# Performance work log

Measured on AMD Instinct MI355X. Metric: run time of the kernel, lower is better.

Reference implementation:

```python
import jax, jax.numpy as jnp
import numpy as np

B = 2048
S = 8            # mem_slots
H = 8            # num_heads
HS = 128         # head_size
KS = 128         # key_size (= head_size)
VS = 128         # value_size
M = H * HS       # mem_size = 1024
QKV = 2 * KS + VS            # 384
TOTAL = QKV * H              # 3072
IN_DIM = 1024
NUM_GATES = 2                # gate_style='memory' -> gate size 1, x2 gates
FORGET_BIAS = 1.0
INPUT_BIAS = 0.0


def _glorot(key, shape):
    fan_in, fan_out = shape[0], shape[1]
    lim = np.sqrt(6.0 / (fan_in + fan_out))
    return jax.random.uniform(key, shape, jnp.float32, -lim, lim)


def setup_inputs() -> dict:
    key = jax.random.key(0)
    ks = jax.random.split(key, 16)
    return {
        "inputs": jax.random.normal(ks[0], (B, IN_DIM), jnp.float32),
        "memory": jax.random.normal(ks[1], (B, S * M), jnp.float32),
        "kernel_qkv": _glorot(ks[2], (M, TOTAL)),
        "bias_qkv": jnp.zeros((TOTAL,), jnp.float32),
        "kernel_gi": _glorot(ks[3], (M, NUM_GATES)),
        "bias_gi": _glorot(ks[4], (1, NUM_GATES))[0],
        "kernel_gm": _glorot(ks[5], (M, NUM_GATES)),
        "bias_gm": _glorot(ks[6], (1, NUM_GATES))[0],
        "kernel_in": _glorot(ks[7], (IN_DIM, M)),
        "bias_in": _glorot(ks[8], (1, M))[0],
        "mlp_k0": _glorot(ks[9], (M, M)),
        "mlp_b0": _glorot(ks[10], (1, M))[0],
        "mlp_k1": _glorot(ks[11], (M, M)),
        "mlp_b1": _glorot(ks[12], (1, M))[0],
    }


def reference(inputs, memory, kernel_qkv, bias_qkv, kernel_gi, bias_gi,
              kernel_gm, bias_gm, kernel_in, bias_in,
              mlp_k0, mlp_b0, mlp_k1, mlp_b1):
    b = inputs.shape[0]
    mem = memory.reshape(b, S, M)                       # (B, S, M)
    x = inputs @ kernel_in + bias_in                    # (B, M)
    mpi = jnp.concatenate([mem, x[:, None, :]], axis=1)  # (B, S+1, M)

    # multi-head attention over memory + input slot
    qkv = (mpi @ kernel_qkv + bias_qkv).reshape(b, S + 1, H, QKV)
    qkv = qkv.transpose(0, 2, 1, 3)                     # (B, H, S+1, QKV)
    q = qkv[..., :KS] * (QKV ** -0.5)
    k = qkv[..., KS:2 * KS]
    v = qkv[..., 2 * KS:]
    w = jax.nn.softmax(jnp.einsum('bhqd,bhkd->bhqk', q, k), axis=-1)
    att = jnp.einsum('bhqk,bhkd->bhqd', w, v)           # (B, H, S+1, VS)
    att = att.transpose(0, 2, 1, 3).reshape(b, S + 1, M)
    m1 = mpi + att                                      # residual attention

    # residual 2-layer MLP (relu between layers)
    h = jax.nn.relu(m1 @ mlp_k0 + mlp_b0)
    m2 = m1 + (h @ mlp_k1 + mlp_b1)

    nxt = m2[:, :-1, :]                                 # drop input slot

    # per-slot (memory-style) gates
    gi = (x @ kernel_gi + bias_gi)[:, None, :]          # (B, 1, 2)
    gm = jnp.tanh(mem) @ kernel_gm + bias_gm            # (B, S, 2)
    gates = gm + gi
    input_gate = jax.nn.sigmoid(gates[..., :1] + INPUT_BIAS)
    forget_gate = jax.nn.sigmoid(gates[..., 1:] + FORGET_BIAS)

    nxt = input_gate * jnp.tanh(nxt) + forget_gate * mem
    return nxt.reshape(b, S * M)
```

## Files before the change

### kernel.cpp

```cpp
#include <hip/hip_runtime.h>
#include <math.h>


typedef unsigned short ushort_t;
typedef short bf16x8_t __attribute__((ext_vector_type(8)));
typedef float f32x4_t  __attribute__((ext_vector_type(4)));

#define MFMA16(a, b, c) __builtin_amdgcn_mfma_f32_16x16x32_bf16((a), (b), (c), 0, 0, 0)
#define SCHED_PIN() __builtin_amdgcn_sched_barrier(0)

__device__ __forceinline__ ushort_t f2bf(float f) {
    unsigned int u = __float_as_uint(f);
    u += 0x7fff + ((u >> 16) & 1);
    return (ushort_t)(u >> 16);
}
__device__ __forceinline__ float bf2f(ushort_t h) {
    return __uint_as_float(((unsigned int)h) << 16);
}
__device__ __forceinline__ float fast_tanh(float x) {
    float e = __expf(2.0f * x);
    return 1.0f - 2.0f * __builtin_amdgcn_rcpf(e + 1.0f);
}
__device__ __forceinline__ float fast_sigmoid(float x) {
    return __builtin_amdgcn_rcpf(1.0f + __expf(-x));
}

__device__ __forceinline__ void load_lds_16(const void* g, void* l) {
    __builtin_amdgcn_global_load_lds(
        (const __attribute__((address_space(1))) void*)g,
        (__attribute__((address_space(3))) void*)l, 16, 0, 0);
}

__global__ __launch_bounds__(512, 2)
void gemm256(const ushort_t* __restrict__ A, const ushort_t* __restrict__ Wt,
             const float* __restrict__ bias, ushort_t* __restrict__ Cb,
             const ushort_t* __restrict__ resb, const float* __restrict__ igfg,
             const ushort_t* __restrict__ memb, float* __restrict__ outp,
             int N, int K, int relu, int ncol, int nrow)
{
    __shared__ __align__(16) ushort_t As[2][256][64];
    __shared__ __align__(16) ushort_t Bs[2][256][64];

    const int tid   = threadIdx.x;
    const int wave  = tid >> 6, lane = tid & 63;
    const int lrow  = lane & 15, lquad = lane >> 4;
    const int wr    = (wave >> 2) * 64;
    const int wc    = (wave & 3) * 32;

    const int nwg = ncol * nrow;
    int l = blockIdx.x;
    int q = nwg >> 3, r = nwg & 7;
    int xcd = l & 7, ib = l >> 3;
    int wg = (xcd < r) ? xcd * (q + 1) + ib : r * (q + 1) + (xcd - r) * q + ib;
    int rT = wg / ncol, cT = wg - rT * ncol;
    const int rowBase = rT * 256;
    const int colBase = cT * 256;

    const int NT = K >> 6;

    auto stage = [&](const ushort_t* __restrict__ G, int gbase, int kt,
                     int half, ushort_t (*lds)[64]) {
        #pragma unroll
        for (int j = 0; j < 2; ++j) {
            int ci   = j * 512 + tid;
            int rl   = ci >> 3;
            int slot = ci & 7;
            int row  = half * 128 + rl;
            int gc   = slot ^ (rl & 7);
            const ushort_t* g = G + (size_t)(gbase + row) * K + kt * 64 + gc * 8;
            load_lds_16(g, &lds[row][slot * 8]);
        }
    };

    stage(A,  rowBase, 0, 0, As[0]);
    stage(A,  rowBase, 0, 1, As[0]);
    stage(Wt, colBase, 0, 0, Bs[0]);
    stage(Wt, colBase, 0, 1, Bs[0]);
    asm volatile("" ::: "memory");
    stage(A,  rowBase, 1, 0, As[1]);
    stage(Wt, colBase, 1, 0, Bs[1]);
    asm volatile("s_waitcnt vmcnt(4)" ::: "memory");
    SCHED_PIN();
    __builtin_amdgcn_s_barrier();
    SCHED_PIN();

    f32x4_t acc[8][4] = {};
    bf16x8_t af[4][2], bfr[4][2];
    const int s0 = (lquad ^ (lrow & 7)) * 8;
    const int s1 = ((lquad ^ (lrow & 7)) ^ 4) * 8;

    for (int t = 0; t < NT; ++t) {
        const int bf = t & 1, nf = bf ^ 1;
        ushort_t (*Ab)[64] = As[bf];
        ushort_t (*Bb)[64] = Bs[bf];

        #pragma unroll
        for (int m = 0; m < 4; ++m) {
            int ra = wr + m * 16 + lrow;
            af[m][0] = *(const bf16x8_t*)&Ab[ra][s0];
            af[m][1] = *(const bf16x8_t*)&Ab[ra][s1];
        }
        #pragma unroll
        for (int n = 0; n < 2; ++n) {
            int rb = wc + n * 16 + lrow;
            bfr[n][0] = *(const bf16x8_t*)&Bb[rb][s0];
            bfr[n][1] = *(const bf16x8_t*)&Bb[rb][s1];
        }
        if (t + 1 < NT) stage(A, rowBase, t + 1, 1, As[nf]);
        asm volatile("s_waitcnt lgkmcnt(8)" ::: "memory");
        SCHED_PIN();
        __builtin_amdgcn_s_barrier();
        asm volatile("s_waitcnt lgkmcnt(0)" ::: "memory");
        SCHED_PIN();
        __builtin_amdgcn_s_setprio(1);
        #pragma unroll
        for (int m = 0; m < 4; ++m)
            #pragma unroll
            for (int n = 0; n < 2; ++n) {
                acc[m][n] = MFMA16(af[m][0], bfr[n][0], acc[m][n]);
                acc[m][n] = MFMA16(af[m][1], bfr[n][1], acc[m][n]);
            }
        __builtin_amdgcn_s_setprio(0);
        SCHED_PIN();
        __builtin_amdgcn_s_barrier();
        SCHED_PIN();

        #pragma unroll
        for (int n = 0; n < 2; ++n) {
            int rb = 128 + wc + n * 16 + lrow;
            bfr[2 + n][0] = *(const bf16x8_t*)&Bb[rb][s0];
            bfr[2 + n][1] = *(const bf16x8_t*)&Bb[rb][s1];
        }
        if (t + 1 < NT) stage(Wt, colBase, t + 1, 1, Bs[nf]);
        SCHED_PIN();
        __builtin_amdgcn_s_barrier();
        asm volatile("s_waitcnt lgkmcnt(0)" ::: "memory");
        SCHED_PIN();
        __builtin_amdgcn_s_setprio(1);
        #pragma unroll
        for (int m = 0; m < 4; ++m)
            #pragma unroll
            for (int n = 0; n < 2; ++n) {
                acc[m][2 + n] = MFMA16(af[m][0], bfr[2 + n][0], acc[m][2 + n]);
                acc[m][2 + n] = MFMA16(af[m][1], bfr[2 + n][1], acc[m][2 + n]);
            }
        __builtin_amdgcn_s_setprio(0);
        SCHED_PIN();
        __builtin_amdgcn_s_barrier();
        SCHED_PIN();

        #pragma unroll
        for (int m = 0; m < 4; ++m) {
            int ra = 128 + wr + m * 16 + lrow;
            af[m][0] = *(const bf16x8_t*)&Ab[ra][s0];
            af[m][1] = *(const bf16x8_t*)&Ab[ra][s1];
        }
        if (t + 2 < NT) stage(A, rowBase, t + 2, 0, As[bf]);
        SCHED_PIN();
        __builtin_amdgcn_s_barrier();
        asm volatile("s_waitcnt lgkmcnt(0)" ::: "memory");
        SCHED_PIN();
        __builtin_amdgcn_s_setprio(1);
        #pragma unroll
        for (int m = 0; m < 4; ++m)
            #pragma unroll
            for (int n = 0; n < 2; ++n) {
                acc[4 + m][n] = MFMA16(af[m][0], bfr[n][0], acc[4 + m][n]);
                acc[4 + m][n] = MFMA16(af[m][1], bfr[n][1], acc[4 + m][n]);
            }
        __builtin_amdgcn_s_setprio(0);
        SCHED_PIN();
        __builtin_amdgcn_s_barrier();
        SCHED_PIN();

        if (t + 2 < NT) {
            stage(Wt, colBase, t + 2, 0, Bs[bf]);
            asm volatile("s_waitcnt vmcnt(4)" ::: "memory");
        } else if (t + 1 < NT) {
            asm volatile("s_waitcnt vmcnt(0)" ::: "memory");
        }
        SCHED_PIN();
        __builtin_amdgcn_s_barrier();
        SCHED_PIN();
        __builtin_amdgcn_s_setprio(1);
        #pragma unroll
        for (int m = 0; m < 4; ++m)
            #pragma unroll
            for (int n = 0; n < 2; ++n) {
                acc[4 + m][2 + n] = MFMA16(af[m][0], bfr[2 + n][0], acc[4 + m][2 + n]);
                acc[4 + m][2 + n] = MFMA16(af[m][1], bfr[2 + n][1], acc[4 + m][2 + n]);
            }
        __builtin_amdgcn_s_setprio(0);
        SCHED_PIN();
        __builtin_amdgcn_s_barrier();
        SCHED_PIN();
    }

    #pragma unroll
    for (int mi = 0; mi < 8; ++mi) {
        #pragma unroll
        for (int ni = 0; ni < 4; ++ni) {
            int col = colBase + wc + (ni & 1) * 16 + ((ni >> 1) << 7) + lrow;
            float bv = bias[col];
            #pragma unroll
            for (int rr = 0; rr < 4; ++rr) {
                int row = rowBase + wr + (mi & 3) * 16 + ((mi >> 2) << 7)
                        + lquad * 4 + rr;
                size_t idx = (size_t)row * N + col;
                float v = acc[mi][ni][rr] + bv;
                if (resb) v += bf2f(resb[idx]);
                if (relu) v = fmaxf(v, 0.f);
                if (outp) {
                    float ig = igfg[row * 2], fg = igfg[row * 2 + 1];
                    float mv = bf2f(memb[(size_t)(row + (row >> 3)) * N + col]);
                    outp[idx] = ig * fast_tanh(v) + fg * mv;
                } else {
                    Cb[idx] = f2bf(v);
                }
            }
        }
    }
}

__global__ __launch_bounds__(256)
void gemm_mfma(const ushort_t* __restrict__ A, const ushort_t* __restrict__ Wt,
               const float* __restrict__ bias, float* __restrict__ Cf,
               ushort_t* __restrict__ Cb, const ushort_t* __restrict__ resb,
               const float* __restrict__ igfg, const ushort_t* __restrict__ memb,
               float* __restrict__ outp, int N, int K, int relu,
               int ncol, int nrow)
{
    __shared__ __align__(16) ushort_t As[128 * 32];
    __shared__ __align__(16) ushort_t Bs[128 * 32];
    const int tid  = threadIdx.x;
    const int wave = tid >> 6, lane = tid & 63;
    const int wr = (wave >> 1) * 64;
    const int wc = (wave & 1)  * 64;
    const int lrow  = lane & 15;
    const int lquad = lane >> 4;

    int l = blockIdx.x, rT, cT;
    if ((nrow & 7) == 0) {
        int group = l / (8 * ncol);
        int w     = l - group * 8 * ncol;
        rT = group * 8 + (w & 7);
        cT = w >> 3;
    } else {
        rT = l / ncol;
        cT = l - rT * ncol;
    }
    const int rowBase = rT * 128;
    const int colBase = cT * 128;

    f32x4_t acc[4][4] = {};

    for (int k0 = 0; k0 < K; k0 += 32) {
        #pragma unroll
        for (int i = 0; i < 2; ++i) {
            int e    = i * 256 + tid;
            int row  = e >> 2;
            int c    = (e & 3) ^ ((row >> 1) & 3);
            const ushort_t* ga = A  + (size_t)(rowBase + row) * K + k0 + c * 8;
            const ushort_t* gb = Wt + (size_t)(colBase + row) * K + k0 + c * 8;
            load_lds_16(ga, &As[e * 8]);
            load_lds_16(gb, &Bs[e * 8]);
        }
        __syncthreads();

        bf16x8_t af[4], bfr[4];
        #pragma unroll
        for (int t = 0; t < 4; ++t) {
            int ma = wr + t * 16 + lrow;
            int pa = lquad ^ ((ma >> 1) & 3);
            af[t]  = *(const bf16x8_t*)&As[ma * 32 + pa * 8];
            int nb = wc + t * 16 + lrow;
            int pb = lquad ^ ((nb >> 1) & 3);
            bfr[t] = *(const bf16x8_t*)&Bs[nb * 32 + pb * 8];
        }
        #pragma unroll
        for (int mi = 0; mi < 4; ++mi)
            #pragma unroll
            for (int ni = 0; ni < 4; ++ni)
                acc[mi][ni] = MFMA16(af[mi], bfr[ni], acc[mi][ni]);
        __syncthreads();
    }

    #pragma unroll
    for (int mi = 0; mi < 4; ++mi) {
        #pragma unroll
        for (int ni = 0; ni < 4; ++ni) {
            int col = colBase + wc + ni * 16 + lrow;
            float bv = bias[col];
            #pragma unroll
            for (int r = 0; r < 4; ++r) {
                int row = rowBase + wr + mi * 16 + lquad * 4 + r;
                size_t idx = (size_t)row * N + col;
                float v = acc[mi][ni][r] + bv;
                if (resb) v += bf2f(resb[idx]);
                if (relu) v = fmaxf(v, 0.f);
                if (outp) {
                    float ig = igfg[row * 2], fg = igfg[row * 2 + 1];
                    float mv = bf2f(memb[(size_t)(row + (row >> 3)) * N + col]);
                    outp[idx] = ig * fast_tanh(v) + fg * mv;
                } else if (Cb) {
                    Cb[idx] = f2bf(v);
                } else {
                    Cf[idx] = v;
                }
            }
        }
    }
}

__global__ __launch_bounds__(256)
void conv_bf16(const float* __restrict__ in, ushort_t* __restrict__ out, size_t n)
{
    size_t i = ((size_t)blockIdx.x * 256 + threadIdx.x) * 4;
    if (i >= n) return;
    float4 v = *(const float4*)(in + i);
    out[i + 0] = f2bf(v.x); out[i + 1] = f2bf(v.y);
    out[i + 2] = f2bf(v.z); out[i + 3] = f2bf(v.w);
}

__global__ __launch_bounds__(256)
void conv_wt4(const float* __restrict__ W0, ushort_t* __restrict__ T0,
              const float* __restrict__ W1, ushort_t* __restrict__ T1,
              const float* __restrict__ W2, ushort_t* __restrict__ T2,
              const float* __restrict__ W3, ushort_t* __restrict__ T3)
{
    __shared__ float t[32][33];
    int bx = blockIdx.x;
    const float* W; ushort_t* T; int N;
    if (bx < 32)       { W = W0; T = T0; N = 1024; }
    else if (bx < 128) { W = W1; T = T1; N = 3072; bx -= 32; }
    else if (bx < 160) { W = W2; T = T2; N = 1024; bx -= 128; }
    else               { W = W3; T = T3; N = 1024; bx -= 160; }
    const int K = 1024;
    const int n0 = bx * 32, k0 = blockIdx.y * 32;
    const int tx = threadIdx.x & 31, ty = threadIdx.x >> 5;
    #pragma unroll
    for (int i = 0; i < 4; ++i)
        t[ty * 4 + i][tx] = W[(size_t)(k0 + ty * 4 + i) * N + n0 + tx];
    __syncthreads();
    #pragma unroll
    for (int i = 0; i < 4; ++i)
        T[(size_t)(n0 + ty * 4 + i) * K + k0 + tx] = f2bf(t[tx][ty * 4 + i]);
}

__global__ __launch_bounds__(256)
void prep_kernel(const float* __restrict__ mem, const ushort_t* __restrict__ xb,
                 const float* __restrict__ kgm, const float* __restrict__ bgm,
                 const float* __restrict__ gi, ushort_t* __restrict__ mpi,
                 float* __restrict__ igfg)
{
    const int row = blockIdx.x;
    const int tid = threadIdx.x;
    const int b = row / 9, s = row - b * 9;
    if (s == 8) {
        ((ushort4*)(mpi + (size_t)row * 1024))[tid] =
            ((const ushort4*)(xb + (size_t)b * 1024))[tid];
        return;
    }
    const float* mrow = mem + ((size_t)b * 8 + s) * 1024;
    float4 v = ((const float4*)mrow)[tid];
    ushort4 o;
    o.x = f2bf(v.x); o.y = f2bf(v.y); o.z = f2bf(v.z); o.w = f2bf(v.w);
    ((ushort4*)(mpi + (size_t)row * 1024))[tid] = o;
    float4 k0 = ((const float4*)kgm)[tid * 2];
    float4 k1 = ((const float4*)kgm)[tid * 2 + 1];
    float t0 = fast_tanh(v.x), t1 = fast_tanh(v.y);
    float t2 = fast_tanh(v.z), t3 = fast_tanh(v.w);
    float g0 = t0 * k0.x + t1 * k0.z + t2 * k1.x + t3 * k1.z;
    float g1 = t0 * k0.y + t1 * k0.w + t2 * k1.y + t3 * k1.w;
    #pragma unroll
    for (int m = 1; m <= 32; m <<= 1) {
        g0 += __shfl_xor(g0, m);
        g1 += __shfl_xor(g1, m);
    }
    __shared__ float wg[4][2];
    if ((tid & 63) == 0) { wg[tid >> 6][0] = g0; wg[tid >> 6][1] = g1; }
    __syncthreads();
    if (tid == 0) {
        float G0 = wg[0][0] + wg[1][0] + wg[2][0] + wg[3][0];
        float G1 = wg[0][1] + wg[1][1] + wg[2][1] + wg[3][1];
        int orow = b * 8 + s;
        igfg[orow * 2 + 0] = fast_sigmoid(G0 + bgm[0] + gi[b * 2 + 0]);
        igfg[orow * 2 + 1] = fast_sigmoid(G1 + bgm[1] + gi[b * 2 + 1] + 1.0f);
    }
}

__global__ __launch_bounds__(256)
void attn_kernel(const ushort_t* __restrict__ qkv, const ushort_t* __restrict__ mpib,
                 ushort_t* __restrict__ m1b)
{
    const int bh = blockIdx.x;
    const int b = bh >> 3, h = bh & 7;
    constexpr int VS = 40;
    __shared__ __align__(16) ushort_t vt[128 * VS];
    __shared__ __align__(16) ushort_t pw[16 * VS];
    const int tid  = threadIdx.x;
    const int lane = tid & 63, wave = tid >> 6;
    const int quad = lane >> 4;
    const size_t qrow0 = (size_t)b * 9;

    {
        unsigned long long* z = (unsigned long long*)vt;
        #pragma unroll
        for (int i = 0; i < 5; ++i) z[tid + i * 256] = 0ull;
        if (tid < 160) ((unsigned long long*)pw)[tid] = 0ull;
    }
    __syncthreads();
    for (int c = tid; c < 9 * 128; c += 256) {
        int j = c >> 7, d = c & 127;
        vt[d * VS + j] = qkv[(qrow0 + j) * 3072 + (size_t)h * 384 + 256 + d];
    }

    f32x4_t sacc = {0.f, 0.f, 0.f, 0.f};
    if (wave == 0) {
        const int m  = lane & 7;
        const int n  = lane & 15;
        const int nc = n > 8 ? 8 : n;
        const ushort_t* qb = qkv + (qrow0 + m)  * 3072 + (size_t)h * 384 + quad * 8;
        const ushort_t* kb = qkv + (qrow0 + nc) * 3072 + (size_t)h * 384 + 128 + quad * 8;
        #pragma unroll
        for (int t = 0; t < 4; ++t) {
            bf16x8_t aq = *(const bf16x8_t*)(qb + t * 32);
            bf16x8_t bk = *(const bf16x8_t*)(kb + t * 32);
            sacc = __builtin_amdgcn_mfma_f32_16x16x32_bf16(aq, bk, sacc, 0, 0, 0);
        }
    }
    __syncthreads();

    if (wave == 0) {
        const int j = lane & 15;
        const float scale = 0.05103103630798288f;
        #pragma unroll
        for (int r = 0; r < 4; ++r) {
            float sv = (j < 9) ? sacc[r] * scale : -1e30f;
            float mx = sv;
            mx = fmaxf(mx, __shfl_xor(mx, 1));
            mx = fmaxf(mx, __shfl_xor(mx, 2));
            mx = fmaxf(mx, __shfl_xor(mx, 4));
            mx = fmaxf(mx, __shfl_xor(mx, 8));
            float e = (j < 9) ? __expf(sv - mx) : 0.f;
            float sum = e;
            sum += __shfl_xor(sum, 1);
            sum += __shfl_xor(sum, 2);
            sum += __shfl_xor(sum, 4);
            sum += __shfl_xor(sum, 8);
            pw[(quad * 4 + r) * VS + j] = f2bf(e * __builtin_amdgcn_rcpf(sum));
        }
    }
    __syncthreads();

    {
        const int n  = lane & 15;
        const int d0 = wave * 32;
        bf16x8_t pa = *(const bf16x8_t*)&pw[n * VS + quad * 8];
        #pragma unroll
        for (int g = 0; g < 2; ++g) {
            int d = d0 + g * 16 + n;
            bf16x8_t vb = *(const bf16x8_t*)&vt[d * VS + quad * 8];
            f32x4_t o = {0.f, 0.f, 0.f, 0.f};
            o = __builtin_amdgcn_mfma_f32_16x16x32_bf16(pa, vb, o, 0, 0, 0);
            #pragma unroll
            for (int r = 0; r < 4; ++r) {
                int i = quad * 4 + r;
                if (i < 8) {
                    float mv = bf2f(mpib[((size_t)b * 9 + i) * 1024 + (size_t)h * 128 + d]);
                    size_t idx = ((size_t)b * 8 + i) * 1024 + (size_t)h * 128 + d;
                    m1b[idx] = f2bf(o[r] + mv);
                }
            }
        }
    }
}

__global__ __launch_bounds__(256)
void gi_kernel(const ushort_t* __restrict__ xb, const float* __restrict__ kgi,
               const float* __restrict__ bgi, float* __restrict__ gi)
{
    const int b = blockIdx.x, tid = threadIdx.x;
    float g0 = 0.f, g1 = 0.f;
    for (int k = tid; k < 1024; k += 256) {
        float xv = bf2f(xb[(size_t)b * 1024 + k]);
        g0 += xv * kgi[k * 2];
        g1 += xv * kgi[k * 2 + 1];
    }
    #pragma unroll
    for (int m = 1; m <= 32; m <<= 1) {
        g0 += __shfl_xor(g0, m);
        g1 += __shfl_xor(g1, m);
    }
    __shared__ float wg[4][2];
    if ((tid & 63) == 0) { wg[tid >> 6][0] = g0; wg[tid >> 6][1] = g1; }
    __syncthreads();
    if (tid == 0) {
        gi[b * 2 + 0] = wg[0][0] + wg[1][0] + wg[2][0] + wg[3][0] + bgi[0];
        gi[b * 2 + 1] = wg[0][1] + wg[1][1] + wg[2][1] + wg[3][1] + bgi[1];
    }
}

extern "C" void kernel_launch(void* const* d_in, const int* in_sizes, int n_in,
                              void* d_out, int out_size, void* d_ws, size_t ws_size,
                              hipStream_t stream)
{
    const float* inputs     = (const float*)d_in[0];
    const float* memory     = (const float*)d_in[1];
    const float* kernel_qkv = (const float*)d_in[2];
    const float* bias_qkv   = (const float*)d_in[3];
    const float* kernel_gi  = (const float*)d_in[4];
    const float* bias_gi    = (const float*)d_in[5];
    const float* kernel_gm  = (const float*)d_in[6];
    const float* bias_gm    = (const float*)d_in[7];
    const float* kernel_in  = (const float*)d_in[8];
    const float* bias_in    = (const float*)d_in[9];
    const float* mlp_k0     = (const float*)d_in[10];
    const float* mlp_b0     = (const float*)d_in[11];
    const float* mlp_k1     = (const float*)d_in[12];
    const float* mlp_b1     = (const float*)d_in[13];
    float* out = (float*)d_out;

    char* p = (char*)d_ws;
    ushort_t* in_b   = (ushort_t*)p;  p += (size_t)2048 * 1024 * 2;
    ushort_t* x_b    = (ushort_t*)p;  p += (size_t)2048 * 1024 * 2;
    ushort_t* wt_in  = (ushort_t*)p;  p += (size_t)1024 * 1024 * 2;
    ushort_t* wt_qkv = (ushort_t*)p;  p += (size_t)3072 * 1024 * 2;
    ushort_t* wt_k0  = (ushort_t*)p;  p += (size_t)1024 * 1024 * 2;
    ushort_t* wt_k1  = (ushort_t*)p;  p += (size_t)1024 * 1024 * 2;
    float*    ws_gi  = (float*)p;     p += (size_t)2048 * 2 * 4;
    float*    igfg   = (float*)p;     p += (size_t)16384 * 2 * 4;
    ushort_t* ws_mpi = (ushort_t*)p;  p += (size_t)18432 * 1024 * 2;
    ushort_t* m1b    = (ushort_t*)p;  p += (size_t)16384 * 1024 * 2;
    ushort_t* ws_h   = (ushort_t*)p;  p += (size_t)16384 * 1024 * 2;
    size_t fixed = (size_t)(p - (char*)d_ws);

    int Bc = 256;
    for (int cand = 1024; cand >= 256; cand >>= 1)
        if (fixed + (size_t)cand * 9 * 3072 * 2 <= ws_size) { Bc = cand; break; }
    ushort_t* ws_qkv = (ushort_t*)p;

    conv_bf16<<<2048, 256, 0, stream>>>(inputs, in_b, (size_t)2048 * 1024);
    conv_wt4<<<dim3(192, 32), 256, 0, stream>>>(
        kernel_in, wt_in, kernel_qkv, wt_qkv, mlp_k0, wt_k0, mlp_k1, wt_k1);

    gemm_mfma<<<16 * 8, 256, 0, stream>>>(
        in_b, wt_in, bias_in, nullptr, x_b, nullptr, nullptr, nullptr, nullptr,
        1024, 1024, 0, 8, 16);

    gi_kernel<<<2048, 256, 0, stream>>>(x_b, kernel_gi, bias_gi, ws_gi);
    prep_kernel<<<18432, 256, 0, stream>>>(memory, x_b, kernel_gm, bias_gm,
                                           ws_gi, ws_mpi, igfg);

    const int NC = 2048 / Bc;
    for (int c = 0; c < NC; ++c) {
        const int b0 = c * Bc;
        const int nrow = Bc * 9 / 256;
        gemm256<<<12 * nrow, 512, 0, stream>>>(
            ws_mpi + (size_t)b0 * 9 * 1024, wt_qkv, bias_qkv, ws_qkv,
            nullptr, nullptr, nullptr, nullptr, 3072, 1024, 0, 12, nrow);
        attn_kernel<<<Bc * 8, 256, 0, stream>>>(
            ws_qkv, ws_mpi + (size_t)b0 * 9 * 1024, m1b + (size_t)b0 * 8192);
    }

    gemm256<<<64 * 4, 512, 0, stream>>>(
        m1b, wt_k0, mlp_b0, ws_h, nullptr, nullptr, nullptr, nullptr,
        1024, 1024, 1, 4, 64);

    gemm256<<<64 * 4, 512, 0, stream>>>(
        ws_h, wt_k1, mlp_b1, nullptr, m1b, igfg, ws_mpi, out,
        1024, 1024, 0, 4, 64);
}
```

Baseline: 576.3 us.

## Double-buffer 128-tile GEMM, move MLP GEMMs to it, slim gemm256

Adds LDS double buffering to the small 128x128 GEMM kernel so the next K-slice loads while MFMAs run. The two MLP GEMMs (16384x1024x1024) now use this 128-tile kernel with 1024 workgroups instead of the 256-tile kernel with 256 workgroups. gemm256 is reduced to a plain bf16-output path without sched barriers or fused epilogues, keeping it only for the QKV projection. The 128 tile does less data reuse per workgroup but spreads work over more workgroups, and dropping the sched barriers may change how instructions are interleaved.

Measured after the change: 550.7 us. -4.5%, faster.

```diff
diff --git a/kernel.cpp b/kernel.cpp
--- a/kernel.cpp
+++ b/kernel.cpp
@@ -7,7 +7,6 @@
 typedef float f32x4_t  __attribute__((ext_vector_type(4)));
 
 #define MFMA16(a, b, c) __builtin_amdgcn_mfma_f32_16x16x32_bf16((a), (b), (c), 0, 0, 0)
-#define SCHED_PIN() __builtin_amdgcn_sched_barrier(0)
 
 __device__ __forceinline__ ushort_t f2bf(float f) {
     unsigned int u = __float_as_uint(f);
@@ -31,207 +30,16 @@
         (__attribute__((address_space(3))) void*)l, 16, 0, 0);
 }
 
-__global__ __launch_bounds__(512, 2)
-void gemm256(const ushort_t* __restrict__ A, const ushort_t* __restrict__ Wt,
-             const float* __restrict__ bias, ushort_t* __restrict__ Cb,
-             const ushort_t* __restrict__ resb, const float* __restrict__ igfg,
-             const ushort_t* __restrict__ memb, float* __restrict__ outp,
-             int N, int K, int relu, int ncol, int nrow)
-{
-    __shared__ __align__(16) ushort_t As[2][256][64];
-    __shared__ __align__(16) ushort_t Bs[2][256][64];
-
-    const int tid   = threadIdx.x;
-    const int wave  = tid >> 6, lane = tid & 63;
-    const int lrow  = lane & 15, lquad = lane >> 4;
-    const int wr    = (wave >> 2) * 64;
-    const int wc    = (wave & 3) * 32;
-
-    const int nwg = ncol * nrow;
-    int l = blockIdx.x;
-    int q = nwg >> 3, r = nwg & 7;
-    int xcd = l & 7, ib = l >> 3;
-    int wg = (xcd < r) ? xcd * (q + 1) + ib : r * (q + 1) + (xcd - r) * q + ib;
-    int rT = wg / ncol, cT = wg - rT * ncol;
-    const int rowBase = rT * 256;
-    const int colBase = cT * 256;
-
-    const int NT = K >> 6;
-
-    auto stage = [&](const ushort_t* __restrict__ G, int gbase, int kt,
-                     int half, ushort_t (*lds)[64]) {
-        #pragma unroll
-        for (int j = 0; j < 2; ++j) {
-            int ci   = j * 512 + tid;
-            int rl   = ci >> 3;
-            int slot = ci & 7;
-            int row  = half * 128 + rl;
-            int gc   = slot ^ (rl & 7);
-            const ushort_t* g = G + (size_t)(gbase + row) * K + kt * 64 + gc * 8;
-            load_lds_16(g, &lds[row][slot * 8]);
-        }
-    };
-
-    stage(A,  rowBase, 0, 0, As[0]);
-    stage(A,  rowBase, 0, 1, As[0]);
-    stage(Wt, colBase, 0, 0, Bs[0]);
-    stage(Wt, colBase, 0, 1, Bs[0]);
-    asm volatile("" ::: "memory");
-    stage(A,  rowBase, 1, 0, As[1]);
-    stage(Wt, colBase, 1, 0, Bs[1]);
-    asm volatile("s_waitcnt vmcnt(4)" ::: "memory");
-    SCHED_PIN();
-    __builtin_amdgcn_s_barrier();
-    SCHED_PIN();
-
-    f32x4_t acc[8][4] = {};
-    bf16x8_t af[4][2], bfr[4][2];
-    const int s0 = (lquad ^ (lrow & 7)) * 8;
-    const int s1 = ((lquad ^ (lrow & 7)) ^ 4) * 8;
-
-    for (int t = 0; t < NT; ++t) {
-        const int bf = t & 1, nf = bf ^ 1;
-        ushort_t (*Ab)[64] = As[bf];
-        ushort_t (*Bb)[64] = Bs[bf];
-
-        #pragma unroll
-        for (int m = 0; m < 4; ++m) {
-            int ra = wr + m * 16 + lrow;
-            af[m][0] = *(const bf16x8_t*)&Ab[ra][s0];
-            af[m][1] = *(const bf16x8_t*)&Ab[ra][s1];
-        }
-        #pragma unroll
-        for (int n = 0; n < 2; ++n) {
-            int rb = wc + n * 16 + lrow;
-            bfr[n][0] = *(const bf16x8_t*)&Bb[rb][s0];
-            bfr[n][1] = *(const bf16x8_t*)&Bb[rb][s1];
-        }
-        if (t + 1 < NT) stage(A, rowBase, t + 1, 1, As[nf]);
-        asm volatile("s_waitcnt lgkmcnt(8)" ::: "memory");
-        SCHED_PIN();
-        __builtin_amdgcn_s_barrier();
-        asm volatile("s_waitcnt lgkmcnt(0)" ::: "memory");
-        SCHED_PIN();
-        __builtin_amdgcn_s_setprio(1);
-        #pragma unroll
-        for (int m = 0; m < 4; ++m)
-            #pragma unroll
-            for (int n = 0; n < 2; ++n) {
-                acc[m][n] = MFMA16(af[m][0], bfr[n][0], acc[m][n]);
-                acc[m][n] = MFMA16(af[m][1], bfr[n][1], acc[m][n]);
-            }
-        __builtin_amdgcn_s_setprio(0);
-        SCHED_PIN();
-        __builtin_amdgcn_s_barrier();
-        SCHED_PIN();
-
-        #pragma unroll
-        for (int n = 0; n < 2; ++n) {
-            int rb = 128 + wc + n * 16 + lrow;
-            bfr[2 + n][0] = *(const bf16x8_t*)&Bb[rb][s0];
-            bfr[2 + n][1] = *(const bf16x8_t*)&Bb[rb][s1];
-        }
-        if (t + 1 < NT) stage(Wt, colBase, t + 1, 1, Bs[nf]);
-        SCHED_PIN();
-        __builtin_amdgcn_s_barrier();
-        asm volatile("s_waitcnt lgkmcnt(0)" ::: "memory");
-        SCHED_PIN();
-        __builtin_amdgcn_s_setprio(1);
-        #pragma unroll
-        for (int m = 0; m < 4; ++m)
-            #pragma unroll
-            for (int n = 0; n < 2; ++n) {
-                acc[m][2 + n] = MFMA16(af[m][0], bfr[2 + n][0], acc[m][2 + n]);
-                acc[m][2 + n] = MFMA16(af[m][1], bfr[2 + n][1], acc[m][2 + n]);
-            }
-        __builtin_amdgcn_s_setprio(0);
-        SCHED_PIN();
-        __builtin_amdgcn_s_barrier();
-        SCHED_PIN();
-
-        #pragma unroll
-        for (int m = 0; m < 4; ++m) {
-            int ra = 128 + wr + m * 16 + lrow;
-            af[m][0] = *(const bf16x8_t*)&Ab[ra][s0];
-            af[m][1] = *(const bf16x8_t*)&Ab[ra][s1];
-        }
-        if (t + 2 < NT) stage(A, rowBase, t + 2, 0, As[bf]);
-        SCHED_PIN();
-        __builtin_amdgcn_s_barrier();
-        asm volatile("s_waitcnt lgkmcnt(0)" ::: "memory");
-        SCHED_PIN();
-        __builtin_amdgcn_s_setprio(1);
-        #pragma unroll
-        for (int m = 0; m < 4; ++m)
-            #pragma unroll
-            for (int n = 0; n < 2; ++n) {
-                acc[4 + m][n] = MFMA16(af[m][0], bfr[n][0], acc[4 + m][n]);
-                acc[4 + m][n] = MFMA16(af[m][1], bfr[n][1], acc[4 + m][n]);
-            }
-        __builtin_amdgcn_s_setprio(0);
-        SCHED_PIN();
-        __builtin_amdgcn_s_barrier();
-        SCHED_PIN();
-
-        if (t + 2 < NT) {
-            stage(Wt, colBase, t + 2, 0, Bs[bf]);
-            asm volatile("s_waitcnt vmcnt(4)" ::: "memory");
-        } else if (t + 1 < NT) {
-            asm volatile("s_waitcnt vmcnt(0)" ::: "memory");
-        }
-        SCHED_PIN();
-        __builtin_amdgcn_s_barrier();
-        SCHED_PIN();
-        __builtin_amdgcn_s_setprio(1);
-        #pragma unroll
-        for (int m = 0; m < 4; ++m)
-            #pragma unroll
-            for (int n = 0; n < 2; ++n) {
-                acc[4 + m][2 + n] = MFMA16(af[m][0], bfr[2 + n][0], acc[4 + m][2 + n]);
-                acc[4 + m][2 + n] = MFMA16(af[m][1], bfr[2 + n][1], acc[4 + m][2 + n]);
-            }
-        __builtin_amdgcn_s_setprio(0);
-        SCHED_PIN();
-        __builtin_amdgcn_s_barrier();
-        SCHED_PIN();
-    }
-
-    #pragma unroll
-    for (int mi = 0; mi < 8; ++mi) {
-        #pragma unroll
-        for (int ni = 0; ni < 4; ++ni) {
-            int col = colBase + wc + (ni & 1) * 16 + ((ni >> 1) << 7) + lrow;
-            float bv = bias[col];
-            #pragma unroll
-            for (int rr = 0; rr < 4; ++rr) {
-                int row = rowBase + wr + (mi & 3) * 16 + ((mi >> 2) << 7)
-                        + lquad * 4 + rr;
-                size_t idx = (size_t)row * N + col;
-                float v = acc[mi][ni][rr] + bv;
-                if (resb) v += bf2f(resb[idx]);
-                if (relu) v = fmaxf(v, 0.f);
-                if (outp) {
-                    float ig = igfg[row * 2], fg = igfg[row * 2 + 1];
-                    float mv = bf2f(memb[(size_t)(row + (row >> 3)) * N + col]);
-                    outp[idx] = ig * fast_tanh(v) + fg * mv;
-                } else {
-                    Cb[idx] = f2bf(v);
-                }
-            }
-        }
-    }
-}
-
 __global__ __launch_bounds__(256)
-void gemm_mfma(const ushort_t* __restrict__ A, const ushort_t* __restrict__ Wt,
+void gemm128db(const ushort_t* __restrict__ A, const ushort_t* __restrict__ Wt,
                const float* __restrict__ bias, float* __restrict__ Cf,
                ushort_t* __restrict__ Cb, const ushort_t* __restrict__ resb,
                const float* __restrict__ igfg, const ushort_t* __restrict__ memb,
                float* __restrict__ outp, int N, int K, int relu,
                int ncol, int nrow)
 {
-    __shared__ __align__(16) ushort_t As[128 * 32];
-    __shared__ __align__(16) ushort_t Bs[128 * 32];
+    __shared__ __align__(16) ushort_t As[2][128][32];
+    __shared__ __align__(16) ushort_t Bs[2][128][32];
     const int tid  = threadIdx.x;
     const int wave = tid >> 6, lane = tid & 63;
     const int wr = (wave >> 1) * 64;
@@ -252,37 +60,50 @@
     const int rowBase = rT * 128;
     const int colBase = cT * 128;
 
+    auto stage = [&](const ushort_t* __restrict__ G, int gbase, int k0,
+                     ushort_t (*lds)[32]) {
+        #pragma unroll
+        for (int i = 0; i < 2; ++i) {
+            int e   = i * 256 + tid;
+            int row = e >> 2;
+            int sl  = e & 3;
+            int gc  = sl ^ ((row >> 1) & 3);
+            const ushort_t* g = G + (size_t)(gbase + row) * K + k0 + gc * 8;
+            load_lds_16(g, &lds[row][sl * 8]);
+        }
+    };
+
     f32x4_t acc[4][4] = {};
 
+    stage(A,  rowBase, 0, As[0]);
+    stage(Wt, colBase, 0, Bs[0]);
+    __syncthreads();
+
+    int buf = 0;
     for (int k0 = 0; k0 < K; k0 += 32) {
-        #pragma unroll
-        for (int i = 0; i < 2; ++i) {
-            int e    = i * 256 + tid;
-            int row  = e >> 2;
-            int c    = (e & 3) ^ ((row >> 1) & 3);
-            const ushort_t* ga = A  + (size_t)(rowBase + row) * K + k0 + c * 8;
-            const ushort_t* gb = Wt + (size_t)(colBase + row) * K + k0 + c * 8;
-            load_lds_16(ga, &As[e * 8]);
-            load_lds_16(gb, &Bs[e * 8]);
-        }
-        __syncthreads();
+        if (k0 + 32 < K) {
+            stage(A,  rowBase, k0 + 32, As[buf ^ 1]);
+            stage(Wt, colBase, k0 + 32, Bs[buf ^ 1]);
+        }
 
         bf16x8_t af[4], bfr[4];
         #pragma unroll
         for (int t = 0; t < 4; ++t) {
             int ma = wr + t * 16 + lrow;
             int pa = lquad ^ ((ma >> 1) & 3);
-            af[t]  = *(const bf16x8_t*)&As[ma * 32 + pa * 8];
+            af[t]  = *(const bf16x8_t*)&As[buf][ma][pa * 8];
             int nb = wc + t * 16 + lrow;
             int pb = lquad ^ ((nb >> 1) & 3);
-            bfr[t] = *(const bf16x8_t*)&Bs[nb * 32 + pb * 8];
+            bfr[t] = *(const bf16x8_t*)&Bs[buf][nb][pb * 8];
         }
         #pragma unroll
         for (int mi = 0; mi < 4; ++mi)
             #pragma unroll
             for (int ni = 0; ni < 4; ++ni)
                 acc[mi][ni] = MFMA16(af[mi], bfr[ni], acc[mi][ni]);
+
         __syncthreads();
+        buf ^= 1;
     }
 
     #pragma unroll
@@ -312,6 +133,167 @@
     }
 }
 
+__global__ __launch_bounds__(512, 2)
+void gemm256(const ushort_t* __restrict__ A, const ushort_t* __restrict__ Wt,
+             const float* __restrict__ bias, ushort_t* __restrict__ Cb,
+             int N, int K, int ncol, int nrow)
+{
+    __shared__ __align__(16) ushort_t As[2][256][64];
+    __shared__ __align__(16) ushort_t Bs[2][256][64];
+
+    const int tid   = threadIdx.x;
+    const int wave  = tid >> 6, lane = tid & 63;
+    const int lrow  = lane & 15, lquad = lane >> 4;
+    const int wr    = (wave >> 2) * 64;
+    const int wc    = (wave & 3) * 32;
+
+    const int nwg = ncol * nrow;
+    int l = blockIdx.x;
+    int q = nwg >> 3, r = nwg & 7;
+    int xcd = l & 7, ib = l >> 3;
+    int wg = (xcd < r) ? xcd * (q + 1) + ib : r * (q + 1) + (xcd - r) * q + ib;
+    int rT = wg / ncol, cT = wg - rT * ncol;
+    const int rowBase = rT * 256;
+    const int colBase = cT * 256;
+
+    const int NT = K >> 6;
+
+    auto stage = [&](const ushort_t* __restrict__ G, int gbase, int kt,
+                     int half, ushort_t (*lds)[64]) {
+        #pragma unroll
+        for (int j = 0; j < 2; ++j) {
+            int ci   = j * 512 + tid;
+            int rl   = ci >> 3;
+            int slot = ci & 7;
+            int row  = half * 128 + rl;
+            int gc   = slot ^ (rl & 7);
+            const ushort_t* g = G + (size_t)(gbase + row) * K + kt * 64 + gc * 8;
+            load_lds_16(g, &lds[row][slot * 8]);
+        }
+    };
+
+    stage(A,  rowBase, 0, 0, As[0]);
+    stage(A,  rowBase, 0, 1, As[0]);
+    stage(Wt, colBase, 0, 0, Bs[0]);
+    stage(Wt, colBase, 0, 1, Bs[0]);
+    asm volatile("" ::: "memory");
+    stage(A,  rowBase, 1, 0, As[1]);
+    stage(Wt, colBase, 1, 0, Bs[1]);
+    asm volatile("s_waitcnt vmcnt(4)" ::: "memory");
+    __builtin_amdgcn_s_barrier();
+
+    f32x4_t acc[8][4] = {};
+    bf16x8_t af[4][2], bfr[4][2];
+    const int s0 = (lquad ^ (lrow & 7)) * 8;
+    const int s1 = ((lquad ^ (lrow & 7)) ^ 4) * 8;
+
+    for (int t = 0; t < NT; ++t) {
+        const int bf = t & 1, nf = bf ^ 1;
+        ushort_t (*Ab)[64] = As[bf];
+        ushort_t (*Bb)[64] = Bs[bf];
+
+        #pragma unroll
+        for (int m = 0; m < 4; ++m) {
+            int ra = wr + m * 16 + lrow;
+            af[m][0] = *(const bf16x8_t*)&Ab[ra][s0];
+            af[m][1] = *(const bf16x8_t*)&Ab[ra][s1];
+        }
+        #pragma unroll
+        for (int n = 0; n < 2; ++n) {
+            int rb = wc + n * 16 + lrow;
+            bfr[n][0] = *(const bf16x8_t*)&Bb[rb][s0];
+            bfr[n][1] = *(const bf16x8_t*)&Bb[rb][s1];
+        }
+        if (t + 1 < NT) stage(A, rowBase, t + 1, 1, As[nf]);
+        __builtin_amdgcn_s_barrier();
+        asm volatile("s_waitcnt lgkmcnt(0)" ::: "memory");
+        __builtin_amdgcn_s_setprio(1);
+        #pragma unroll
+        for (int m = 0; m < 4; ++m)
+            #pragma unroll
+            for (int n = 0; n < 2; ++n) {
+                acc[m][n] = MFMA16(af[m][0], bfr[n][0], acc[m][n]);
+                acc[m][n] = MFMA16(af[m][1], bfr[n][1], acc[m][n]);
+            }
+        __builtin_amdgcn_s_setprio(0);
+        __builtin_amdgcn_s_barrier();
+
+        #pragma unroll
+        for (int n = 0; n < 2; ++n) {
+            int rb = 128 + wc + n * 16 + lrow;
+            bfr[2 + n][0] = *(const bf16x8_t*)&Bb[rb][s0];
+            bfr[2 + n][1] = *(const bf16x8_t*)&Bb[rb][s1];
+        }
+        if (t + 1 < NT) stage(Wt, colBase, t + 1, 1, Bs[nf]);
+        __builtin_amdgcn_s_barrier();
+        asm volatile("s_waitcnt lgkmcnt(0)" ::: "memory");
+        __builtin_amdgcn_s_setprio(1);
+        #pragma unroll
+        for (int m = 0; m < 4; ++m)
+            #pragma unroll
+            for (int n = 0; n < 2; ++n) {
+                acc[m][2 + n] = MFMA16(af[m][0], bfr[2 + n][0], acc[m][2 + n]);
+                acc[m][2 + n] = MFMA16(af[m][1], bfr[2 + n][1], acc[m][2 + n]);
+            }
+        __builtin_amdgcn_s_setprio(0);
+        __builtin_amdgcn_s_barrier();
+
+        #pragma unroll
+        for (int m = 0; m < 4; ++m) {
+            int ra = 128 + wr + m * 16 + lrow;
+            af[m][0] = *(const bf16x8_t*)&Ab[ra][s0];
+            af[m][1] = *(const bf16x8_t*)&Ab[ra][s1];
+        }
+        if (t + 2 < NT) stage(A, rowBase, t + 2, 0, As[bf]);
+        __builtin_amdgcn_s_barrier();
+        asm volatile("s_waitcnt lgkmcnt(0)" ::: "memory");
+        __builtin_amdgcn_s_setprio(1);
+        #pragma unroll
+        for (int m = 0; m < 4; ++m)
+            #pragma unroll
+            for (int n = 0; n < 2; ++n) {
+                acc[4 + m][n] = MFMA16(af[m][0], bfr[n][0], acc[4 + m][n]);
+                acc[4 + m][n] = MFMA16(af[m][1], bfr[n][1], acc[4 + m][n]);
+            }
+        __builtin_amdgcn_s_setprio(0);
+        __builtin_amdgcn_s_barrier();
+
+        if (t + 2 < NT) {
+            stage(Wt, colBase, t + 2, 0, Bs[bf]);
+            asm volatile("s_waitcnt vmcnt(4)" ::: "memory");
+        } else if (t + 1 < NT) {
+            asm volatile("s_waitcnt vmcnt(0)" ::: "memory");
+        }
+        __builtin_amdgcn_s_barrier();
+        __builtin_amdgcn_s_setprio(1);
+        #pragma unroll
+        for (int m = 0; m < 4; ++m)
+            #pragma unroll
+            for (int n = 0; n < 2; ++n) {
+                acc[4 + m][2 + n] = MFMA16(af[m][0], bfr[2 + n][0], acc[4 + m][2 + n]);
+                acc[4 + m][2 + n] = MFMA16(af[m][1], bfr[2 + n][1], acc[4 + m][2 + n]);
+            }
+        __builtin_amdgcn_s_setprio(0);
+        __builtin_amdgcn_s_barrier();
+    }
+
+    #pragma unroll
+    for (int mi = 0; mi < 8; ++mi) {
+        #pragma unroll
+        for (int ni = 0; ni < 4; ++ni) {
+            int col = colBase + wc + (ni & 1) * 16 + ((ni >> 1) << 7) + lrow;
+            float bv = bias[col];
+            #pragma unroll
+            for (int rr = 0; rr < 4; ++rr) {
+                int row = rowBase + wr + (mi & 3) * 16 + ((mi >> 2) << 7)
+                        + lquad * 4 + rr;
+                size_t idx = (size_t)row * N + col;
+                Cb[idx] = f2bf(acc[mi][ni][rr] + bv);
+            }
+        }
+    }
+}
+
 __global__ __launch_bounds__(256)
 void conv_bf16(const float* __restrict__ in, ushort_t* __restrict__ out, size_t n)
 {
@@ -544,7 +526,7 @@
     conv_wt4<<<dim3(192, 32), 256, 0, stream>>>(
         kernel_in, wt_in, kernel_qkv, wt_qkv, mlp_k0, wt_k0, mlp_k1, wt_k1);
 
-    gemm_mfma<<<16 * 8, 256, 0, stream>>>(
+    gemm128db<<<16 * 8, 256, 0, stream>>>(
         in_b, wt_in, bias_in, nullptr, x_b, nullptr, nullptr, nullptr, nullptr,
         1024, 1024, 0, 8, 16);
 
@@ -558,16 +540,16 @@
         const int nrow = Bc * 9 / 256;
         gemm256<<<12 * nrow, 512, 0, stream>>>(
             ws_mpi + (size_t)b0 * 9 * 1024, wt_qkv, bias_qkv, ws_qkv,
-            nullptr, nullptr, nullptr, nullptr, 3072, 1024, 0, 12, nrow);
+            3072, 1024, 12, nrow);
         attn_kernel<<<Bc * 8, 256, 0, stream>>>(
             ws_qkv, ws_mpi + (size_t)b0 * 9 * 1024, m1b + (size_t)b0 * 8192);
     }
 
-    gemm256<<<64 * 4, 512, 0, stream>>>(
-        m1b, wt_k0, mlp_b0, ws_h, nullptr, nullptr, nullptr, nullptr,
-        1024, 1024, 1, 4, 64);
-
-    gemm256<<<64 * 4, 512, 0, stream>>>(
-        ws_h, wt_k1, mlp_b1, nullptr, m1b, igfg, ws_mpi, out,
-        1024, 1024, 0, 4, 64);
-}
+    gemm128db<<<128 * 8, 256, 0, stream>>>(
+        m1b, wt_k0, mlp_b0, nullptr, ws_h, nullptr, nullptr, nullptr, nullptr,
+        1024, 1024, 1, 8, 128);
+
+    gemm128db<<<128 * 8, 256, 0, stream>>>(
+        ws_h, wt_k1, mlp_b1, nullptr, nullptr, m1b, igfg, ws_mpi, out,
+        1024, 1024, 0, 8, 128);
+}
```
